# Performance work log

Hardware: AMD Instinct MI355X
Metric: run time of the kernel (lower is better)

## Reference

```python
import jax, jax.numpy as jnp
import numpy as np

H = 1024  # hidden_dim
DT = 0.1
LN_EPS = 1e-5


def setup_inputs() -> dict:
    key = jax.random.key(0)
    ks = jax.random.split(key, 8)
    h = H
    ph = h // 2
    x = jax.random.normal(ks[0], (8, 2048, h), dtype=jnp.float32)
    # S initialized to identity in torch; add small noise so math is non-trivial
    S = jnp.eye(h, dtype=jnp.float32) + 0.02 * jax.random.normal(ks[1], (h, h), dtype=jnp.float32)
    # Hamiltonian MLP: Linear(h,h) -> tanh -> Linear(h,1)
    lim1 = 1.0 / np.sqrt(h)
    W1 = jax.random.uniform(ks[2], (h, h), minval=-lim1, maxval=lim1, dtype=jnp.float32)
    b1 = jax.random.uniform(ks[3], (h,), minval=-lim1, maxval=lim1, dtype=jnp.float32)
    w2 = jax.random.uniform(ks[4], (h,), minval=-lim1, maxval=lim1, dtype=jnp.float32)
    b2 = jax.random.uniform(ks[5], (1,), minval=-lim1, maxval=lim1, dtype=jnp.float32)
    # symplectic structure matrix J (buffer)
    I = jnp.eye(ph, dtype=jnp.float32)
    J = jnp.zeros((h, h), dtype=jnp.float32)
    J = J.at[:ph, ph:].set(I)
    J = J.at[ph:, :ph].set(-I)
    gamma = jnp.ones((h,), dtype=jnp.float32)
    beta = jnp.zeros((h,), dtype=jnp.float32)
    return {"x": x, "S": S, "W1": W1, "b1": b1, "w2": w2, "b2": b2,
            "J": J, "gamma": gamma, "beta": beta, "num_steps": 3}


def reference(x, S, W1, b1, w2, b2, J, gamma, beta, num_steps):
    h = x.shape[-1]
    # Cayley-approx symplectic projection (training branch): S_sym = I + 2*A, A skew part
    A = (S - S.T) * 0.5
    S_sym = jnp.eye(h, dtype=x.dtype) + 2.0 * A
    # z = einsum('ij,...j->...i', S_sym, x)
    z = x @ S_sym.T
    for _ in range(num_steps):
        # analytic grad of H(z) = w2 . tanh(z W1^T + b1) + b2 wrt z
        t = jnp.tanh(z @ W1.T + b1)             # [..., h]
        grad_H = ((1.0 - t * t) * w2) @ W1       # [..., h]
        flow = grad_H @ J.T                      # einsum('ij,...j->...i', J, grad_H)
        z = z + DT * flow
    y = z + x
    # LayerNorm over last dim
    mu = jnp.mean(y, axis=-1, keepdims=True)
    var = jnp.mean((y - mu) ** 2, axis=-1, keepdims=True)
    return (y - mu) * jax.lax.rsqrt(var + LN_EPS) * gamma + beta
```

## Files before the change

kernel.cpp:

```cpp
#include <hip/hip_runtime.h>
#include <hip/hip_bf16.h>

#define H 1024
#define PH 512
#define MROWS 16384
#define DT 0.1f
#define LN_EPS 1e-5f

#define BM 128
#define BN 128
#define BK 64

typedef short s16x8 __attribute__((ext_vector_type(8)));
typedef float f32x4 __attribute__((ext_vector_type(4)));

__device__ __forceinline__ float b2f(short v) {
    union { float f; unsigned u; } c;
    c.u = ((unsigned)(unsigned short)v) << 16;
    return c.f;
}
__device__ __forceinline__ short f2b(float f) {
    union { float f; unsigned u; } c;
    c.f = f;
    unsigned u = c.u;
    unsigned r = u + 0x7FFFu + ((u >> 16) & 1u);
    return (short)(r >> 16);
}
__device__ __forceinline__ float ftanh(float s) {
    float e = __expf(2.0f * s);
    return 1.0f - 2.0f * __builtin_amdgcn_rcpf(e + 1.0f);
}

__global__ __launch_bounds__(256)
void prep_t(const float* __restrict__ S, const float* __restrict__ W1,
            short* __restrict__ Wsym, short* __restrict__ WsymT,
            short* __restrict__ W1b,
            short* __restrict__ Wfd, short* __restrict__ WflowT) {
    __shared__ float T0[64][65];
    __shared__ float T1[64][65];
    __shared__ short Ts[64][66];
    const int I = blockIdx.y * 64, J = blockIdx.x * 64;
    const int c  = threadIdx.x & 63;
    const int r0 = (threadIdx.x >> 6) * 16;
#pragma unroll
    for (int rr = 0; rr < 16; ++rr) {
        int r = r0 + rr;
        T0[r][c] = S[(size_t)(I + r) * H + J + c];
        T1[r][c] = S[(size_t)(J + r) * H + I + c];
    }
    __syncthreads();
    const int pJ = (J + PH) & (H - 1);
    const short sflip = (J >= PH) ? (short)0x8000 : (short)0;
#pragma unroll
    for (int rr = 0; rr < 16; ++rr) {
        int r = r0 + rr;
        size_t rowb = (size_t)(I + r) * H;
        float d = T0[r][c] - T1[c][r];
        Wsym [rowb + J + c] = f2b(d);
        WsymT[rowb + J + c] = f2b(-d);
        W1b  [rowb + J + c] = f2b(W1[rowb + J + c]);
        short wt = (short)(f2b(W1[rowb + pJ + c]) ^ sflip);
        WflowT[rowb + J + c] = wt;
        Ts[r][c] = wt;
    }
    __syncthreads();
#pragma unroll
    for (int rr = 0; rr < 16; ++rr) {
        int r = r0 + rr;
        Wfd[(size_t)(J + r) * H + I + c] = f2b(DT * b2f(Ts[c][r]));
    }
}

__global__ __launch_bounds__(256)
void cvt_x(const float* __restrict__ x, short* __restrict__ xb) {
    int t = blockIdx.x * 256 + threadIdx.x;
    const float4* p = (const float4*)x + (size_t)t * 2;
    float4 f0 = p[0], f1 = p[1];
    s16x8 v;
    v[0] = f2b(f0.x); v[1] = f2b(f0.y); v[2] = f2b(f0.z); v[3] = f2b(f0.w);
    v[4] = f2b(f1.x); v[5] = f2b(f1.y); v[6] = f2b(f1.z); v[7] = f2b(f1.w);
    ((s16x8*)xb)[t] = v;
}

template <int KIND, bool G2D>
__global__ __launch_bounds__(256, 4)
void gemm_k(const short* __restrict__ A, const short* __restrict__ Bw,
            short* __restrict__ out,
            const float* __restrict__ xf,
            const float* __restrict__ w2f,
            const short* __restrict__ u0r,
            const short* __restrict__ pg,
            short* __restrict__ out2,
            const short* __restrict__ A2,
            const short* __restrict__ B2,
            float clampv)
{
    __shared__ short As[BM * BK];
    __shared__ short Bs[BN * BK];

    const int tid  = threadIdx.x;
    const int lane = tid & 63;
    const int wave = tid >> 6;
    const int wm   = wave >> 1;
    const int wn   = wave & 1;

    int m0, n0;
    if (G2D) {
        m0 = blockIdx.y * BM;
        n0 = blockIdx.x * BN;
    } else {
        const int lid   = blockIdx.x;
        const int chunk = ((lid & 7) << 7) | (lid >> 3);
        m0 = (chunk >> 3) * BM;
        n0 = (chunk & 7) * BN;
    }

    const int lrow = lane & 15;
    const int quad = lane >> 4;
    const int swzr = (lrow & 7) << 4;

    const int srow  = lane >> 3;
    const int selem = 8 * ((lane & 7) ^ srow);

    f32x4 acc[4][4] = {};

    const int KSTEPS = (KIND == 7) ? (2 * H / BK) : (H / BK);
    for (int t = 0; t < KSTEPS; ++t) {
        const int k0 = t * BK;
        const short* Au = A;
        const short* Bu = Bw;
        if (KIND == 7 && k0 >= H) { Au = A2; Bu = B2; }
        const int kk = k0 & (H - 1);
#pragma unroll
        for (int i = 0; i < 4; ++i) {
            int ch = wave * 4 + i;
            const short* asrc = Au + (size_t)(m0 + ch * 8 + srow) * H + kk + selem;
            const short* bsrc = Bu + (size_t)(n0 + ch * 8 + srow) * H + kk + selem;
            __builtin_amdgcn_global_load_lds(
                (const __attribute__((address_space(1))) void*)asrc,
                (__attribute__((address_space(3))) void*)(As + ch * 512), 16, 0, 0);
            __builtin_amdgcn_global_load_lds(
                (const __attribute__((address_space(1))) void*)bsrc,
                (__attribute__((address_space(3))) void*)(Bs + ch * 512), 16, 0, 0);
        }
        __syncthreads();

#pragma unroll
        for (int ks = 0; ks < 2; ++ks) {
            s16x8 af[4], bfr[4];
#pragma unroll
            for (int mt = 0; mt < 4; ++mt) {
                int row = wm * 64 + mt * 16 + lrow;
                af[mt] = *(const s16x8*)((const char*)As + row * 128 +
                                         ((ks * 64 + quad * 16) ^ swzr));
            }
#pragma unroll
            for (int nt = 0; nt < 4; ++nt) {
                int col = wn * 64 + nt * 16 + lrow;
                bfr[nt] = *(const s16x8*)((const char*)Bs + col * 128 +
                                          ((ks * 64 + quad * 16) ^ swzr));
            }
#pragma unroll
            for (int mt = 0; mt < 4; ++mt)
#pragma unroll
                for (int nt = 0; nt < 4; ++nt)
                    acc[mt][nt] = __builtin_amdgcn_mfma_f32_16x16x32_bf16(
                        bfr[nt], af[mt], acc[mt][nt], 0, 0, 0);
        }
        __syncthreads();
    }

    float4 bvv[4], wvv[4];
    if (KIND == 1 || KIND == 3 || KIND == 4) {
#pragma unroll
        for (int nt = 0; nt < 4; ++nt) {
            int col = n0 + wn * 64 + nt * 16 + quad * 4;
            bvv[nt] = *(const float4*)(xf + col);
            wvv[nt] = *(const float4*)(w2f + col);
        }
    }
#pragma unroll
    for (int mt = 0; mt < 4; ++mt) {
        const int row = m0 + wm * 64 + mt * 16 + lrow;
        const size_t rbase = (size_t)row * H;
#pragma unroll
        for (int nt = 0; nt < 4; ++nt) {
            const int col = n0 + wn * 64 + nt * 16 + quad * 4;
            const size_t idx = rbase + col;
            f32x4 a = acc[mt][nt];
            short4 o;
            if (KIND == 0) {
                float4 xv = *(const float4*)(xf + idx);
                o.x = f2b(a[0] + xv.x);
                o.y = f2b(a[1] + xv.y);
                o.z = f2b(a[2] + xv.z);
                o.w = f2b(a[3] + xv.w);
                *(short4*)(out + idx) = o;
            } else if (KIND == 1) {
                float t0 = ftanh(a[0] + bvv[nt].x);
                float t1 = ftanh(a[1] + bvv[nt].y);
                float t2 = ftanh(a[2] + bvv[nt].z);
                float t3 = ftanh(a[3] + bvv[nt].w);
                o.x = f2b((1.0f - t0 * t0) * wvv[nt].x);
                o.y = f2b((1.0f - t1 * t1) * wvv[nt].y);
                o.z = f2b((1.0f - t2 * t2) * wvv[nt].z);
                o.w = f2b((1.0f - t3 * t3) * wvv[nt].w);
                *(short4*)(out + idx) = o;
            } else if (KIND == 2) {
                short4 zo = *(const short4*)(out + idx);
                float d0 = fminf(fmaxf(a[0], -clampv), clampv);
                float d1 = fminf(fmaxf(a[1], -clampv), clampv);
                float d2 = fminf(fmaxf(a[2], -clampv), clampv);
                float d3 = fminf(fmaxf(a[3], -clampv), clampv);
                o.x = f2b(b2f(zo.x) + d0);
                o.y = f2b(b2f(zo.y) + d1);
                o.z = f2b(b2f(zo.z) + d2);
                o.w = f2b(b2f(zo.w) + d3);
                *(short4*)(out + idx) = o;
            } else if (KIND == 3) {
                short4 u;
                u.x = f2b(a[0]); u.y = f2b(a[1]); u.z = f2b(a[2]); u.w = f2b(a[3]);
                *(short4*)(out + idx) = u;
                float t0 = ftanh(a[0] + bvv[nt].x);
                float t1 = ftanh(a[1] + bvv[nt].y);
                float t2 = ftanh(a[2] + bvv[nt].z);
                float t3 = ftanh(a[3] + bvv[nt].w);
                o.x = f2b((1.0f - t0 * t0) * wvv[nt].x);
                o.y = f2b((1.0f - t1 * t1) * wvv[nt].y);
                o.z = f2b((1.0f - t2 * t2) * wvv[nt].z);
                o.w = f2b((1.0f - t3 * t3) * wvv[nt].w);
                *(short4*)(out2 + idx) = o;
            } else if (KIND == 4) {
                short4 u4 = *(const short4*)(u0r + idx);
                short4 p4 = *(const short4*)(pg + idx);
                float t0 = ftanh(b2f(u4.x) + a[0] + bvv[nt].x);
                float t1 = ftanh(b2f(u4.y) + a[1] + bvv[nt].y);
                float t2 = ftanh(b2f(u4.z) + a[2] + bvv[nt].z);
                float t3 = ftanh(b2f(u4.w) + a[3] + bvv[nt].w);
                o.x = f2b(b2f(p4.x) + (1.0f - t0 * t0) * wvv[nt].x);
                o.y = f2b(b2f(p4.y) + (1.0f - t1 * t1) * wvv[nt].y);
                o.z = f2b(b2f(p4.z) + (1.0f - t2 * t2) * wvv[nt].z);
                o.w = f2b(b2f(p4.w) + (1.0f - t3 * t3) * wvv[nt].w);
                *(short4*)(out2 + idx) = o;
            } else if (KIND == 5) {
                o.x = f2b(DT * a[0]);
                o.y = f2b(DT * a[1]);
                o.z = f2b(DT * a[2]);
                o.w = f2b(DT * a[3]);
                *(short4*)(out + idx) = o;
            } else {
                o.x = f2b(a[0]);
                o.y = f2b(a[1]);
                o.z = f2b(a[2]);
                o.w = f2b(a[3]);
                *(short4*)(out + idx) = o;
            }
        }
    }
}

__global__ __launch_bounds__(256)
void ln_k(const short* __restrict__ z, const float* __restrict__ x,
          const float* __restrict__ gamma, const float* __restrict__ beta,
          float* __restrict__ out, float xmul) {
    const int row = blockIdx.x;
    const int tid = threadIdx.x;
    const size_t base = (size_t)row * H;
    short4 z4 = ((const short4*)(z + base))[tid];
    float4 x4 = ((const float4*)(x + base))[tid];
    float y0 = fmaf(xmul, x4.x, b2f(z4.x));
    float y1 = fmaf(xmul, x4.y, b2f(z4.y));
    float y2 = fmaf(xmul, x4.z, b2f(z4.z));
    float y3 = fmaf(xmul, x4.w, b2f(z4.w));
    float s = y0 + y1 + y2 + y3;
    float q = y0 * y0 + y1 * y1 + y2 * y2 + y3 * y3;
#pragma unroll
    for (int off = 32; off > 0; off >>= 1) {
        s += __shfl_down(s, off);
        q += __shfl_down(q, off);
    }
    __shared__ float ss[4], qs[4];
    if ((tid & 63) == 0) { ss[tid >> 6] = s; qs[tid >> 6] = q; }
    __syncthreads();
    s = ss[0] + ss[1] + ss[2] + ss[3];
    q = qs[0] + qs[1] + qs[2] + qs[3];
    const float mu  = s * (1.0f / H);
    const float var = q * (1.0f / H) - mu * mu;
    const float rs  = rsqrtf(var + LN_EPS);
    const int col = tid * 4;
    float4 o;
    o.x = (y0 - mu) * rs * gamma[col + 0] + beta[col + 0];
    o.y = (y1 - mu) * rs * gamma[col + 1] + beta[col + 1];
    o.z = (y2 - mu) * rs * gamma[col + 2] + beta[col + 2];
    o.w = (y3 - mu) * rs * gamma[col + 3] + beta[col + 3];
    ((float4*)(out + base))[tid] = o;
}

extern "C" void kernel_launch(void* const* d_in, const int* in_sizes, int n_in,
                              void* d_out, int out_size, void* d_ws, size_t ws_size,
                              hipStream_t stream) {
    int ix = 0;
    for (int i = 0; i < n_in; ++i)
        if (in_sizes[i] == MROWS * H) { ix = i; break; }

    const float *x, *S, *W1, *b1, *w2, *gamma, *beta;
    if (ix == 0) {
        x     = (const float*)d_in[0];
        S     = (const float*)d_in[1];
        W1    = (const float*)d_in[2];
        b1    = (const float*)d_in[3];
        w2    = (const float*)d_in[4];
        gamma = (const float*)d_in[7];
        beta  = (const float*)d_in[8];
    } else {
        S     = (const float*)d_in[1];
        W1    = (const float*)d_in[2];
        b1    = (const float*)d_in[3];
        beta  = (const float*)d_in[5];
        gamma = (const float*)d_in[6];
        w2    = (const float*)d_in[8];
        x     = (const float*)d_in[ix];
    }

    const size_t MB = 1024 * 1024;
    float* out    = (float*)d_out;
    short* u0     = (short*)d_out;
    char*  hi     = (char*)d_out + 32 * MB;
    short* Wsym   = (short*)(hi);
    short* WsymT  = (short*)(hi + 2 * MB);
    short* W1b    = (short*)(hi + 4 * MB);
    short* WflowT = (short*)(hi + 6 * MB);
    short* Wfd    = (short*)(hi + 8 * MB);
    short* Wu     = (short*)(hi + 10 * MB);
    short* GT     = (short*)(hi + 12 * MB);
    short* xb     = (short*)d_ws;
    short* gsumA  = (short*)((char*)d_ws + 32 * MB);
    short* gsumB  = (short*)((char*)d_ws + 64 * MB);
    short* z      = gsumB;

    const bool fast = ws_size >= 96 * MB;
    const int  nblk = (H / BN) * (MROWS / BM);

    prep_t<<<dim3(16, 16), 256, 0, stream>>>(S, W1, Wsym, WsymT, W1b, Wfd, WflowT);

    if (fast) {
        cvt_x<<<(MROWS * H / 8) / 256, 256, 0, stream>>>(x, xb);
        gemm_k<0, true><<<dim3(H / BN, H / BM), 256, 0, stream>>>(
            W1b, WsymT, Wu, W1, nullptr, nullptr, nullptr, nullptr,
            nullptr, nullptr, 0.0f);
        gemm_k<5, true><<<dim3(H / BN, H / BM), 256, 0, stream>>>(
            W1b, WflowT, GT, nullptr, nullptr, nullptr, nullptr, nullptr,
            nullptr, nullptr, 0.0f);
        gemm_k<3, false><<<nblk, 256, 0, stream>>>(
            xb, Wu, u0, b1, w2, nullptr, nullptr, gsumA,
            nullptr, nullptr, 0.0f);
        gemm_k<4, false><<<nblk, 256, 0, stream>>>(
            gsumA, GT, nullptr, b1, w2, u0, gsumA, gsumB,
            nullptr, nullptr, 0.0f);
        gemm_k<4, false><<<nblk, 256, 0, stream>>>(
            gsumB, GT, nullptr, b1, w2, u0, gsumB, gsumA,
            nullptr, nullptr, 0.0f);
        gemm_k<7, false><<<nblk, 256, 0, stream>>>(
            xb, Wsym, z, nullptr, nullptr, nullptr, nullptr, nullptr,
            gsumA, Wfd, 0.0f);
        ln_k<<<MROWS, 256, 0, stream>>>(z, x, gamma, beta, out, 2.0f);
    } else {
        short* xbo = (short*)d_out;
        short* go  = (short*)d_out;
        short* zf  = (short*)d_ws;
        cvt_x<<<(MROWS * H / 8) / 256, 256, 0, stream>>>(x, xbo);
        gemm_k<0, false><<<nblk, 256, 0, stream>>>(
            xbo, Wsym, zf, x, nullptr, nullptr, nullptr, nullptr,
            nullptr, nullptr, 0.0f);
        for (int step = 0; step < 3; ++step) {
            gemm_k<1, false><<<nblk, 256, 0, stream>>>(
                zf, W1b, go, b1, w2, nullptr, nullptr, nullptr,
                nullptr, nullptr, 0.0f);
            gemm_k<2, false><<<nblk, 256, 0, stream>>>(
                go, Wfd, zf, nullptr, nullptr, nullptr, nullptr, nullptr,
                nullptr, nullptr, 0.01f);
        }
        ln_k<<<MROWS, 256, 0, stream>>>(zf, x, gamma, beta, out, 1.0f);
    }
}
```

Baseline: 415.6 us.

## Fuse all stages into one cooperative persistent kernel with grid syncs

Replaces the chain of separate launches (prep, convert, weight GEMMs, three flow GEMMs, final GEMM, layernorm) with a single cooperative kernel of 1024 blocks that separates the stages with grid.sync(). The aim is to remove per-launch overhead and the gaps between kernels. Prep and x conversion now run concurrently in different blocks, and prep reads S directly instead of staging one of its tiles in LDS. The cost is grid-wide barriers and the requirement that all 1024 blocks be co-resident. If the cooperative launch fails, the code falls back to the old multi-kernel path.

```diff
diff --git a/kernel.cpp b/kernel.cpp
--- a/kernel.cpp
+++ b/kernel.cpp
@@ -1,5 +1,8 @@
 #include <hip/hip_runtime.h>
 #include <hip/hip_bf16.h>
+#include <hip/hip_cooperative_groups.h>
+
+namespace cgx = cooperative_groups;
 
 #define H 1024
 #define PH 512
@@ -31,21 +34,18 @@
     return 1.0f - 2.0f * __builtin_amdgcn_rcpf(e + 1.0f);
 }
 
-__global__ __launch_bounds__(256)
-void prep_t(const float* __restrict__ S, const float* __restrict__ W1,
-            short* __restrict__ Wsym, short* __restrict__ WsymT,
-            short* __restrict__ W1b,
-            short* __restrict__ Wfd, short* __restrict__ WflowT) {
-    __shared__ float T0[64][65];
-    __shared__ float T1[64][65];
-    __shared__ short Ts[64][66];
-    const int I = blockIdx.y * 64, J = blockIdx.x * 64;
-    const int c  = threadIdx.x & 63;
-    const int r0 = (threadIdx.x >> 6) * 16;
+
+__device__ __forceinline__ void prep_tile(char* smem,
+        const float* S, const float* W1,
+        short* Wsym, short* WsymT, short* W1b, short* WflowT, short* Wfd,
+        int b, int tid) {
+    float (*T1)[65] = (float (*)[65])smem;
+    short (*Ts)[66] = (short (*)[66])(smem + 64 * 65 * 4);
+    const int I = (b >> 4) * 64, J = (b & 15) * 64;
+    const int c = tid & 63, r0 = (tid >> 6) * 16;
 #pragma unroll
     for (int rr = 0; rr < 16; ++rr) {
         int r = r0 + rr;
-        T0[r][c] = S[(size_t)(I + r) * H + J + c];
         T1[r][c] = S[(size_t)(J + r) * H + I + c];
     }
     __syncthreads();
@@ -55,7 +55,7 @@
     for (int rr = 0; rr < 16; ++rr) {
         int r = r0 + rr;
         size_t rowb = (size_t)(I + r) * H;
-        float d = T0[r][c] - T1[c][r];
+        float d = S[rowb + J + c] - T1[c][r];
         Wsym [rowb + J + c] = f2b(d);
         WsymT[rowb + J + c] = f2b(-d);
         W1b  [rowb + J + c] = f2b(W1[rowb + J + c]);
@@ -71,54 +71,35 @@
     }
 }
 
-__global__ __launch_bounds__(256)
-void cvt_x(const float* __restrict__ x, short* __restrict__ xb) {
-    int t = blockIdx.x * 256 + threadIdx.x;
-    const float4* p = (const float4*)x + (size_t)t * 2;
-    float4 f0 = p[0], f1 = p[1];
-    s16x8 v;
-    v[0] = f2b(f0.x); v[1] = f2b(f0.y); v[2] = f2b(f0.z); v[3] = f2b(f0.w);
-    v[4] = f2b(f1.x); v[5] = f2b(f1.y); v[6] = f2b(f1.z); v[7] = f2b(f1.w);
-    ((s16x8*)xb)[t] = v;
-}
-
-template <int KIND, bool G2D>
-__global__ __launch_bounds__(256, 4)
-void gemm_k(const short* __restrict__ A, const short* __restrict__ Bw,
-            short* __restrict__ out,
-            const float* __restrict__ xf,
-            const float* __restrict__ w2f,
-            const short* __restrict__ u0r,
-            const short* __restrict__ pg,
-            short* __restrict__ out2,
-            const short* __restrict__ A2,
-            const short* __restrict__ B2,
-            float clampv)
-{
-    __shared__ short As[BM * BK];
-    __shared__ short Bs[BN * BK];
-
-    const int tid  = threadIdx.x;
+__device__ __forceinline__ void cvt_piece(const float* x, short* xb, int b, int tid) {
+    const int N8 = MROWS * H / 8;
+    for (int t = (b - 256) * 256 + tid; t < N8; t += 768 * 256) {
+        const float4* p = (const float4*)x + (size_t)t * 2;
+        float4 f0 = p[0], f1 = p[1];
+        s16x8 v;
+        v[0] = f2b(f0.x); v[1] = f2b(f0.y); v[2] = f2b(f0.z); v[3] = f2b(f0.w);
+        v[4] = f2b(f1.x); v[5] = f2b(f1.y); v[6] = f2b(f1.z); v[7] = f2b(f1.w);
+        ((s16x8*)xb)[t] = v;
+    }
+}
+
+template <int KIND>
+__device__ __forceinline__ void gemm_core(char* smem,
+        const short* A, const short* Bw, short* out,
+        const float* xf, const float* w2f,
+        const short* u0r, const short* pg, short* out2,
+        const short* A2, const short* B2,
+        int m0, int n0, int tid, float clampv) {
+    short* As = (short*)smem;
+    short* Bs = (short*)(smem + 16384);
+
     const int lane = tid & 63;
     const int wave = tid >> 6;
     const int wm   = wave >> 1;
     const int wn   = wave & 1;
-
-    int m0, n0;
-    if (G2D) {
-        m0 = blockIdx.y * BM;
-        n0 = blockIdx.x * BN;
-    } else {
-        const int lid   = blockIdx.x;
-        const int chunk = ((lid & 7) << 7) | (lid >> 3);
-        m0 = (chunk >> 3) * BM;
-        n0 = (chunk & 7) * BN;
-    }
-
     const int lrow = lane & 15;
     const int quad = lane >> 4;
     const int swzr = (lrow & 7) << 4;
-
     const int srow  = lane >> 3;
     const int selem = 8 * ((lane & 7) ^ srow);
 
@@ -259,12 +240,11 @@
     }
 }
 
-__global__ __launch_bounds__(256)
-void ln_k(const short* __restrict__ z, const float* __restrict__ x,
-          const float* __restrict__ gamma, const float* __restrict__ beta,
-          float* __restrict__ out, float xmul) {
-    const int row = blockIdx.x;
-    const int tid = threadIdx.x;
+__device__ __forceinline__ void ln_row(char* smem,
+        const short* z, const float* x, const float* gamma, const float* beta,
+        float* out, int row, int tid, float xmul) {
+    float* ss = (float*)smem;
+    float* qs = ss + 4;
     const size_t base = (size_t)row * H;
     short4 z4 = ((const short4*)(z + base))[tid];
     float4 x4 = ((const float4*)(x + base))[tid];
@@ -279,7 +259,7 @@
         s += __shfl_down(s, off);
         q += __shfl_down(q, off);
     }
-    __shared__ float ss[4], qs[4];
+    __syncthreads();
     if ((tid & 63) == 0) { ss[tid >> 6] = s; qs[tid >> 6] = q; }
     __syncthreads();
     s = ss[0] + ss[1] + ss[2] + ss[3];
@@ -294,6 +274,100 @@
     o.z = (y2 - mu) * rs * gamma[col + 2] + beta[col + 2];
     o.w = (y3 - mu) * rs * gamma[col + 3] + beta[col + 3];
     ((float4*)(out + base))[tid] = o;
+}
+
+__global__ __launch_bounds__(256, 4)
+void mega_k(const float* S, const float* W1, const float* x,
+            const float* b1, const float* w2,
+            const float* gamma, const float* beta,
+            short* Wsym, short* WsymT, short* W1b, short* WflowT, short* Wfd,
+            short* Wu, short* GT, short* xb, short* u0,
+            short* gsumA, short* gsumB, float* out) {
+    __shared__ __align__(16) char smem[32768];
+    const int b = blockIdx.x, tid = threadIdx.x;
+    cgx::grid_group grid = cgx::this_grid();
+
+    if (b < 256) prep_tile(smem, S, W1, Wsym, WsymT, W1b, WflowT, Wfd, b, tid);
+    else         cvt_piece(x, xb, b, tid);
+    grid.sync();
+
+    if (b < 64) {
+        gemm_core<0>(smem, W1b, WsymT, Wu, W1, nullptr, nullptr, nullptr, nullptr,
+                     nullptr, nullptr, (b >> 3) * BM, (b & 7) * BN, tid, 0.0f);
+    } else if (b < 128) {
+        int bb = b - 64;
+        gemm_core<5>(smem, W1b, WflowT, GT, nullptr, nullptr, nullptr, nullptr,
+                     nullptr, nullptr, nullptr, (bb >> 3) * BM, (bb & 7) * BN, tid, 0.0f);
+    }
+    grid.sync();
+
+    const int chunk = ((b & 7) << 7) | (b >> 3);
+    const int m0 = (chunk >> 3) * BM;
+    const int n0 = (chunk & 7) * BN;
+
+    gemm_core<3>(smem, xb, Wu, u0, b1, w2, nullptr, nullptr, gsumA,
+                 nullptr, nullptr, m0, n0, tid, 0.0f);
+    grid.sync();
+    gemm_core<4>(smem, gsumA, GT, nullptr, b1, w2, u0, gsumA, gsumB,
+                 nullptr, nullptr, m0, n0, tid, 0.0f);
+    grid.sync();
+    gemm_core<4>(smem, gsumB, GT, nullptr, b1, w2, u0, gsumB, gsumA,
+                 nullptr, nullptr, m0, n0, tid, 0.0f);
+    grid.sync();
+    gemm_core<7>(smem, xb, Wsym, gsumB, nullptr, nullptr, nullptr, nullptr, nullptr,
+                 gsumA, Wfd, m0, n0, tid, 0.0f);
+    grid.sync();
+    for (int r = 0; r < 16; ++r)
+        ln_row(smem, gsumB, x, gamma, beta, out, b * 16 + r, tid, 2.0f);
+}
+
+__global__ __launch_bounds__(256)
+void prep_k(const float* __restrict__ S, const float* __restrict__ W1,
+            short* __restrict__ Wsym, short* __restrict__ WsymT,
+            short* __restrict__ W1b, short* __restrict__ WflowT,
+            short* __restrict__ Wfd) {
+    __shared__ __align__(16) char smem[32768];
+    prep_tile(smem, S, W1, Wsym, WsymT, W1b, WflowT, Wfd, blockIdx.x, threadIdx.x);
+}
+
+__global__ __launch_bounds__(256)
+void cvt_x(const float* __restrict__ x, short* __restrict__ xb) {
+    int t = blockIdx.x * 256 + threadIdx.x;
+    const float4* p = (const float4*)x + (size_t)t * 2;
+    float4 f0 = p[0], f1 = p[1];
+    s16x8 v;
+    v[0] = f2b(f0.x); v[1] = f2b(f0.y); v[2] = f2b(f0.z); v[3] = f2b(f0.w);
+    v[4] = f2b(f1.x); v[5] = f2b(f1.y); v[6] = f2b(f1.z); v[7] = f2b(f1.w);
+    ((s16x8*)xb)[t] = v;
+}
+
+template <int KIND, bool G2D>
+__global__ __launch_bounds__(256, 4)
+void gemm_k(const short* A, const short* Bw, short* out,
+            const float* xf, const float* w2f,
+            const short* u0r, const short* pg, short* out2,
+            const short* A2, const short* B2, float clampv) {
+    __shared__ __align__(16) char smem[32768];
+    int m0, n0;
+    if (G2D) {
+        m0 = blockIdx.y * BM;
+        n0 = blockIdx.x * BN;
+    } else {
+        const int lid   = blockIdx.x;
+        const int chunk = ((lid & 7) << 7) | (lid >> 3);
+        m0 = (chunk >> 3) * BM;
+        n0 = (chunk & 7) * BN;
+    }
+    gemm_core<KIND>(smem, A, Bw, out, xf, w2f, u0r, pg, out2, A2, B2,
+                    m0, n0, threadIdx.x, clampv);
+}
+
+__global__ __launch_bounds__(256)
+void ln_k(const short* __restrict__ z, const float* __restrict__ x,
+          const float* __restrict__ gamma, const float* __restrict__ beta,
+          float* __restrict__ out, float xmul) {
+    __shared__ __align__(16) char smem[64];
+    ln_row(smem, z, x, gamma, beta, out, blockIdx.x, threadIdx.x, xmul);
 }
 
 extern "C" void kernel_launch(void* const* d_in, const int* in_sizes, int n_in,
@@ -341,7 +415,21 @@
     const bool fast = ws_size >= 96 * MB;
     const int  nblk = (H / BN) * (MROWS / BM);
 
-    prep_t<<<dim3(16, 16), 256, 0, stream>>>(S, W1, Wsym, WsymT, W1b, Wfd, WflowT);
+    if (fast) {
+        void* args[] = {
+            (void*)&S, (void*)&W1, (void*)&x, (void*)&b1, (void*)&w2,
+            (void*)&gamma, (void*)&beta,
+            (void*)&Wsym, (void*)&WsymT, (void*)&W1b, (void*)&WflowT, (void*)&Wfd,
+            (void*)&Wu, (void*)&GT, (void*)&xb, (void*)&u0,
+            (void*)&gsumA, (void*)&gsumB, (void*)&out
+        };
+        hipError_t e = hipLaunchCooperativeKernel(
+            reinterpret_cast<void*>(mega_k), dim3(1024), dim3(256), args, 0, stream);
+        if (e == hipSuccess) return;
+        (void)hipGetLastError();
+    }
+
+    prep_k<<<256, 256, 0, stream>>>(S, W1, Wsym, WsymT, W1b, WflowT, Wfd);
 
     if (fast) {
         cvt_x<<<(MROWS * H / 8) / 256, 256, 0, stream>>>(x, xb);
```

Result: slower. 1.238 ms (+197.9%).
